# Optimization experiments

Hardware: AMD Instinct MI355X
Metric: run time of the kernel (lower is better)

The kernel has to match this reference:

```python
import jax, jax.numpy as jnp
import numpy as np

B, S, E, H = 2, 2048, 1024, 16
DH = E // H  # 64


def setup_inputs() -> dict:
    key = jax.random.key(0)
    ks = jax.random.split(key, 9)
    sc = 1.0 / np.sqrt(E)
    return {
        "x": jax.random.normal(ks[0], (B, S, E), dtype=jnp.float32),
        "Wq": jax.random.normal(ks[1], (E, E), dtype=jnp.float32) * sc,
        "bq": jax.random.normal(ks[2], (E,), dtype=jnp.float32) * 0.02,
        "Wk": jax.random.normal(ks[3], (E, E), dtype=jnp.float32) * sc,
        "bk": jax.random.normal(ks[4], (E,), dtype=jnp.float32) * 0.02,
        "Wv": jax.random.normal(ks[5], (E, E), dtype=jnp.float32) * sc,
        "bv": jax.random.normal(ks[6], (E,), dtype=jnp.float32) * 0.02,
        "Wo": jax.random.normal(ks[7], (E, E), dtype=jnp.float32) * sc,
        "bo": jax.random.normal(ks[8], (E,), dtype=jnp.float32) * 0.02,
    }


def reference(x, Wq, bq, Wk, bk, Wv, bv, Wo, bo):
    b, s, e = x.shape
    h, dh = H, e // H
    # NOTE: original torch code does .view(B, H, S, Dh) on the [B, S, E]
    # projection WITHOUT transposing first; we replicate that exact reshape.
    q = (x @ Wq.T + bq).reshape(b, h, s, dh)
    k = (x @ Wk.T + bk).reshape(b, h, s, dh)
    v = (x @ Wv.T + bv).reshape(b, h, s, dh)
    scale = 1.0 / jnp.sqrt(jnp.asarray(dh, dtype=x.dtype))
    scores = jax.nn.softmax(jnp.einsum("bhqd,bhkd->bhqk", q, k) * scale, axis=-1)
    out = jnp.einsum("bhqk,bhkd->bhqd", scores, v)  # [B,H,S,Dh]
    out = out.transpose(0, 2, 1, 3).reshape(b, s, e)  # matches torch transpose(1,2).view
    return out @ Wo.T + bo
```

## Files before the change

### kernel.cpp

```cpp
#include <hip/hip_runtime.h>
#include <hip/hip_bf16.h>
#include <stdint.h>

typedef __bf16 bf16x8 __attribute__((ext_vector_type(8)));
typedef float  f32x4  __attribute__((ext_vector_type(4)));
typedef float  f32x16 __attribute__((ext_vector_type(16)));
typedef __hip_bfloat16 bf16;

__device__ __forceinline__ void gll16(const void* g, void* l) {
    typedef const unsigned int __attribute__((address_space(1)))* gp_t;
    typedef unsigned int __attribute__((address_space(3)))* lp_t;
    __builtin_amdgcn_global_load_lds((gp_t)(g), (lp_t)(l), 16, 0, 0);
}

__device__ __forceinline__ float fexp2(float x) {
#if __has_builtin(__builtin_amdgcn_exp2f)
    return __builtin_amdgcn_exp2f(x);
#else
    float r; asm volatile("v_exp_f32 %0, %1" : "=v"(r) : "v"(x)); return r;
#endif
}

__global__ __launch_bounds__(256) void prep_convert(
    const float* __restrict__ x,
    const float* __restrict__ wq, const float* __restrict__ wk,
    const float* __restrict__ wv, const float* __restrict__ wo,
    bf16* __restrict__ Xb, bf16* __restrict__ Wcat, bf16* __restrict__ Wob)
{
    int i = blockIdx.x * blockDim.x + threadIdx.x;
    int base = i * 4;
    const float* src; bf16* dst;
    if      (base < 4194304) { src = x  + base;             dst = Xb   + base; }
    else if (base < 5242880) { src = wq + (base - 4194304); dst = Wcat + (base - 4194304); }
    else if (base < 6291456) { src = wk + (base - 5242880); dst = Wcat + 1048576 + (base - 5242880); }
    else if (base < 7340032) { src = wv + (base - 6291456); dst = Wcat + 2097152 + (base - 6291456); }
    else                     { src = wo + (base - 7340032); dst = Wob  + (base - 7340032); }
    float4 v = *(const float4*)src;
    union { bf16 h[4]; ushort4 u; } cv;
    cv.h[0] = __float2bfloat16(v.x);
    cv.h[1] = __float2bfloat16(v.y);
    cv.h[2] = __float2bfloat16(v.z);
    cv.h[3] = __float2bfloat16(v.w);
    *(ushort4*)dst = cv.u;
}

__global__ __launch_bounds__(256, 2) void gemm_qkv(
    const bf16* __restrict__ X, const bf16* __restrict__ Wc,
    const float* __restrict__ bq, const float* __restrict__ bk, const float* __restrict__ bv,
    bf16* __restrict__ Pq, bf16* __restrict__ Pk, bf16* __restrict__ Pv)
{
    __shared__ __align__(16) bf16 Ab[128 * 32];
    __shared__ __align__(16) bf16 Bb[128 * 32];
    const int t = threadIdx.x;
    const int lane = t & 63, w = t >> 6;
    const int lr = lane & 15, lg = lane >> 4;
    const int wr = w >> 1, wc = w & 1;
    const int row0 = blockIdx.y * 128, col0 = blockIdx.x * 128;

    f32x4 acc[4][4] = {};

    const char* Xc  = (const char*)X;
    const char* Wcc = (const char*)Wc;
    char* AbC = (char*)Ab;
    char* BbC = (char*)Bb;
    const int o0 = t * 16, o1 = o0 + 4096;
    const int ldsoff = w * 1024;

    for (int k0 = 0; k0 < 1024; k0 += 32) {
        __syncthreads();
        gll16(Xc  + (size_t)(row0 + (o0 >> 6)) * 2048 + (size_t)k0 * 2 + (o0 & 63), AbC + ldsoff);
        gll16(Wcc + (size_t)(col0 + (o0 >> 6)) * 2048 + (size_t)k0 * 2 + (o0 & 63), BbC + ldsoff);
        gll16(Xc  + (size_t)(row0 + (o1 >> 6)) * 2048 + (size_t)k0 * 2 + (o1 & 63), AbC + 4096 + ldsoff);
        gll16(Wcc + (size_t)(col0 + (o1 >> 6)) * 2048 + (size_t)k0 * 2 + (o1 & 63), BbC + 4096 + ldsoff);
        __syncthreads();
        bf16x8 af[4], bw[4];
        #pragma unroll
        for (int i = 0; i < 4; ++i)
            af[i] = *(const bf16x8*)(AbC + ((wr * 64 + i * 16 + lr) * 32 + lg * 8) * 2);
        #pragma unroll
        for (int j = 0; j < 4; ++j)
            bw[j] = *(const bf16x8*)(BbC + ((wc * 64 + j * 16 + lr) * 32 + lg * 8) * 2);
        #pragma unroll
        for (int i = 0; i < 4; ++i)
            #pragma unroll
            for (int j = 0; j < 4; ++j)
                acc[i][j] = __builtin_amdgcn_mfma_f32_16x16x32_bf16(af[i], bw[j], acc[i][j], 0, 0, 0);
    }

    const int mid = col0 >> 10;
    const float* bias = (mid == 0) ? bq : (mid == 1 ? bk : bv);
    bf16* Out = (mid == 0) ? Pq : (mid == 1 ? Pk : Pv);
    const float scale = (mid == 0) ? 0.125f * 1.44269504f : 1.0f;
    const int nc0 = col0 - (mid << 10) + wc * 64;
    const int mr0 = row0 + wr * 64;
    #pragma unroll
    for (int i = 0; i < 4; ++i)
        #pragma unroll
        for (int j = 0; j < 4; ++j) {
            int cc = nc0 + j * 16 + lr;
            float bsv = bias[cc];
            #pragma unroll
            for (int p = 0; p < 4; ++p) {
                int rr = mr0 + i * 16 + lg * 4 + p;
                Out[(size_t)rr * 1024 + cc] = __float2bfloat16((acc[i][j][p] + bsv) * scale);
            }
        }
}

__global__ __launch_bounds__(256) void transpose_v(const bf16* __restrict__ Pv, bf16* __restrict__ Vt)
{
    __shared__ bf16 tile[64][72];
    const int head = blockIdx.y;
    const int st   = blockIdx.x;
    const bf16* src = Pv + (size_t)head * 131072 + (size_t)st * 4096;
    bf16* dst = Vt + (size_t)head * 131072 + (size_t)st * 64;
    const int t = threadIdx.x;
    const int rr = t >> 2, c0 = (t & 3) * 16;
    #pragma unroll
    for (int u = 0; u < 2; ++u) {
        bf16x8 v = *(const bf16x8*)(src + rr * 64 + c0 + u * 8);
        #pragma unroll
        for (int e = 0; e < 8; ++e) tile[rr][c0 + u * 8 + e] = ((const bf16*)&v)[e];
    }
    __syncthreads();
    #pragma unroll
    for (int u = 0; u < 2; ++u) {
        bf16 ov[8];
        #pragma unroll
        for (int e = 0; e < 8; ++e) {
            int y = u * 8 + e;
            int z = (y & 3) | ((y & 8) >> 1) | ((y & 4) << 1);
            ov[e] = tile[c0 + z][rr];
        }
        *(bf16x8*)(dst + (size_t)rr * 2048 + c0 + u * 8) = *(const bf16x8*)ov;
    }
}

__global__ __launch_bounds__(256, 2) void attn_fwd(
    const bf16* __restrict__ Pq, const bf16* __restrict__ Pk,
    const bf16* __restrict__ Vt, bf16* __restrict__ Of)
{
    __shared__ __align__(16) bf16 Kl[2][128 * 64];
    __shared__ __align__(16) bf16 Vl[2][64 * 128];

    const int blk = blockIdx.x;
    const int head = blk >> 4;
    const int qt = blk & 15;
    const int bb = head >> 4, hh = head & 15;
    const bf16* Qh = Pq + (size_t)head * 131072;
    const char* Khc = (const char*)(Pk + (size_t)head * 131072);
    const char* Vhc = (const char*)(Vt + (size_t)head * 131072);

    const int t = threadIdx.x;
    const int lane = t & 63, w = t >> 6;
    const int ql = lane & 31, hi = lane >> 5;
    const int q0 = qt * 128 + w * 32;

    bf16x8 qf[4];
    #pragma unroll
    for (int m = 0; m < 4; ++m)
        qf[m] = *(const bf16x8*)(Qh + (size_t)(q0 + ql) * 64 + m * 16 + hi * 8);

    f32x16 acc[2] = {};
    float m_run = -1e30f, l_run = 0.f;

    const int stg_o   = t * 16;
    const int stg_key = stg_o >> 7, stg_ks = (stg_o >> 4) & 7;
    const int stg_d   = stg_o >> 8, stg_vs = (stg_o >> 4) & 15;
    const size_t kgo = (size_t)stg_key * 128 + ((stg_ks ^ (stg_key & 7)) * 16);
    const size_t vgo = (size_t)stg_d * 4096 + ((stg_vs ^ (stg_d & 7)) * 16);
    const int ldst = w * 1024;

#define STAGE(S0, BUF)                                                          \
    {                                                                           \
        char* KB = (char*)(Kl[BUF]);                                            \
        char* VB = (char*)(Vl[BUF]);                                            \
        _Pragma("unroll")                                                       \
        for (int qq = 0; qq < 4; ++qq) {                                        \
            gll16(Khc + (size_t)(S0) * 128 + (size_t)qq * 4096 + kgo,           \
                  KB + qq * 4096 + ldst);                                       \
            gll16(Vhc + (size_t)(S0) * 2 + (size_t)qq * 65536 + vgo,            \
                  VB + qq * 4096 + ldst);                                       \
        }                                                                       \
    }

    STAGE(0, 0);
    __syncthreads();

    int cur = 0;
    for (int s0 = 0; s0 < 2048; s0 += 128) {
        if (s0 + 128 < 2048) STAGE(s0 + 128, cur ^ 1);

        const char* KlC = (const char*)(Kl[cur]);
        const char* VlC = (const char*)(Vl[cur]);

        f32x16 sa[4] = {};
        __builtin_amdgcn_s_setprio(1);
        #pragma unroll
        for (int kb = 0; kb < 4; ++kb) {
            int row = kb * 32 + ql;
            #pragma unroll
            for (int m = 0; m < 4; ++m) {
                int byt = row * 128 + ((32 * m + 16 * hi) ^ ((row & 7) << 4));
                bf16x8 kf = *(const bf16x8*)(KlC + byt);
                sa[kb] = __builtin_amdgcn_mfma_f32_32x32x16_bf16(kf, qf[m], sa[kb], 0, 0, 0);
            }
        }
        __builtin_amdgcn_s_setprio(0);

        float mx = -1e30f;
        #pragma unroll
        for (int kb = 0; kb < 4; ++kb)
            #pragma unroll
            for (int r = 0; r < 16; ++r) mx = fmaxf(mx, sa[kb][r]);
        mx = fmaxf(mx, __shfl_xor(mx, 32));
        float mn = fmaxf(m_run, mx);
        float al = fexp2(m_run - mn);
        m_run = mn;
        float rs = 0.f;
        #pragma unroll
        for (int kb = 0; kb < 4; ++kb)
            #pragma unroll
            for (int r = 0; r < 16; ++r) {
                float p = fexp2(sa[kb][r] - mn);
                sa[kb][r] = p;
                rs += p;
            }
        rs += __shfl_xor(rs, 32);
        l_run = l_run * al + rs;
        #pragma unroll
        for (int r = 0; r < 16; ++r) { acc[0][r] *= al; acc[1][r] *= al; }

        __builtin_amdgcn_s_setprio(1);
        #pragma unroll
        for (int sb = 0; sb < 8; ++sb) {
            const int kb = sb >> 1, par = (sb & 1) * 8;
            bf16x8 pa;
            #pragma unroll
            for (int e = 0; e < 8; ++e) pa[e] = (__bf16)sa[kb][par + e];
            #pragma unroll
            for (int db = 0; db < 2; ++db) {
                int row = db * 32 + ql;
                int byt = row * 256 + ((sb * 32 + hi * 16) ^ ((row & 7) << 4));
                bf16x8 vf = *(const bf16x8*)(VlC + byt);
                acc[db] = __builtin_amdgcn_mfma_f32_32x32x16_bf16(vf, pa, acc[db], 0, 0, 0);
            }
        }
        __builtin_amdgcn_s_setprio(0);

        __syncthreads();
        cur ^= 1;
    }
#undef STAGE

    float inv = 1.0f / l_run;
    bf16* orow = Of + (size_t)(bb * 2048 + q0 + ql) * 1024 + hh * 64;
    #pragma unroll
    for (int db = 0; db < 2; ++db)
        #pragma unroll
        for (int g = 0; g < 4; ++g) {
            union { bf16 h[4]; ushort4 u; } ob;
            #pragma unroll
            for (int j = 0; j < 4; ++j)
                ob.h[j] = __float2bfloat16(acc[db][4 * g + j] * inv);
            *(ushort4*)(orow + db * 32 + 8 * g + 4 * hi) = ob.u;
        }
}

__global__ __launch_bounds__(256, 2) void gemm_out(
    const bf16* __restrict__ A, const bf16* __restrict__ W,
    const float* __restrict__ bo, float* __restrict__ C)
{
    __shared__ __align__(16) bf16 Ab[128 * 32];
    __shared__ __align__(16) bf16 Bb[128 * 32];
    const int t = threadIdx.x;
    const int lane = t & 63, w = t >> 6;
    const int lr = lane & 15, lg = lane >> 4;
    const int wr = w >> 1, wc = w & 1;
    const int row0 = blockIdx.y * 128, col0 = blockIdx.x * 128;

    f32x4 acc[4][4] = {};
    const char* Ac = (const char*)A;
    const char* Wc = (const char*)W;
    char* AbC = (char*)Ab;
    char* BbC = (char*)Bb;
    const int o0 = t * 16, o1 = o0 + 4096;
    const int ldsoff = w * 1024;

    for (int k0 = 0; k0 < 1024; k0 += 32) {
        __syncthreads();
        gll16(Ac + (size_t)(row0 + (o0 >> 6)) * 2048 + (size_t)k0 * 2 + (o0 & 63), AbC + ldsoff);
        gll16(Wc + (size_t)(col0 + (o0 >> 6)) * 2048 + (size_t)k0 * 2 + (o0 & 63), BbC + ldsoff);
        gll16(Ac + (size_t)(row0 + (o1 >> 6)) * 2048 + (size_t)k0 * 2 + (o1 & 63), AbC + 4096 + ldsoff);
        gll16(Wc + (size_t)(col0 + (o1 >> 6)) * 2048 + (size_t)k0 * 2 + (o1 & 63), BbC + 4096 + ldsoff);
        __syncthreads();
        bf16x8 af[4], bw[4];
        #pragma unroll
        for (int i = 0; i < 4; ++i)
            af[i] = *(const bf16x8*)(AbC + ((wr * 64 + i * 16 + lr) * 32 + lg * 8) * 2);
        #pragma unroll
        for (int j = 0; j < 4; ++j)
            bw[j] = *(const bf16x8*)(BbC + ((wc * 64 + j * 16 + lr) * 32 + lg * 8) * 2);
        #pragma unroll
        for (int i = 0; i < 4; ++i)
            #pragma unroll
            for (int j = 0; j < 4; ++j)
                acc[i][j] = __builtin_amdgcn_mfma_f32_16x16x32_bf16(af[i], bw[j], acc[i][j], 0, 0, 0);
    }

    const int nc0 = col0 + wc * 64;
    const int mr0 = row0 + wr * 64;
    #pragma unroll
    for (int i = 0; i < 4; ++i)
        #pragma unroll
        for (int j = 0; j < 4; ++j) {
            int cc = nc0 + j * 16 + lr;
            float bsv = bo[cc];
            #pragma unroll
            for (int p = 0; p < 4; ++p) {
                int rr = mr0 + i * 16 + lg * 4 + p;
                C[(size_t)rr * 1024 + cc] = acc[i][j][p] + bsv;
            }
        }
}

extern "C" void kernel_launch(void* const* d_in, const int* in_sizes, int n_in,
                              void* d_out, int out_size, void* d_ws, size_t ws_size,
                              hipStream_t stream) {
    const float* x  = (const float*)d_in[0];
    const float* Wq = (const float*)d_in[1];
    const float* bq = (const float*)d_in[2];
    const float* Wk = (const float*)d_in[3];
    const float* bk = (const float*)d_in[4];
    const float* Wv = (const float*)d_in[5];
    const float* bv = (const float*)d_in[6];
    const float* Wo = (const float*)d_in[7];
    const float* bo = (const float*)d_in[8];
    float* out = (float*)d_out;

    char* ws = (char*)d_ws;
    bf16* Xb   = (bf16*)(ws + 0);
    bf16* Wcat = (bf16*)(ws + 8388608);
    bf16* Wob  = (bf16*)(ws + 14680064);
    bf16* Pq   = (bf16*)(ws + 16777216);
    bf16* Pk   = (bf16*)(ws + 25165824);
    bf16* Pv   = (bf16*)(ws + 33554432);
    bf16* Vt   = (bf16*)(ws + 0);
    bf16* Of   = (bf16*)(ws + 33554432);
    (void)ws_size; (void)in_sizes; (void)n_in; (void)out_size;

    prep_convert<<<8192, 256, 0, stream>>>(x, Wq, Wk, Wv, Wo, Xb, Wcat, Wob);
    gemm_qkv<<<dim3(24, 32), 256, 0, stream>>>(Xb, Wcat, bq, bk, bv, Pq, Pk, Pv);
    transpose_v<<<dim3(32, 32), 256, 0, stream>>>(Pv, Vt);
    attn_fwd<<<512, 256, 0, stream>>>(Pq, Pk, Vt, Of);
    gemm_out<<<dim3(8, 32), 256, 0, stream>>>(Of, Wob, bo, out);
}
```

Before: 125.8 us.

## Remap block IDs for XCD locality and add lazy softmax rescaling

Linear block IDs are remapped so consecutive tiles land on the same XCD (stride-8 interleave) in the QKV GEMM, the attention kernel and the output GEMM. This is meant to improve L2 reuse of shared A/B tiles and K/V heads. The attention softmax also uses tree reductions for max and sum, and skips rescaling the running max and accumulator unless the new max exceeds the old one by more than 8 (log2 units). That removes per-tile exp and multiply work, at the risk of larger unnormalized values within the bounded threshold.

```diff
diff --git a/kernel.cpp b/kernel.cpp
--- a/kernel.cpp
+++ b/kernel.cpp
@@ -19,6 +19,24 @@
 #else
     float r; asm volatile("v_exp_f32 %0, %1" : "=v"(r) : "v"(x)); return r;
 #endif
+}
+
+__device__ __forceinline__ float tmax16(const f32x16& v) {
+    float a0 = fmaxf(v[0], v[1]),   a1 = fmaxf(v[2], v[3]);
+    float a2 = fmaxf(v[4], v[5]),   a3 = fmaxf(v[6], v[7]);
+    float a4 = fmaxf(v[8], v[9]),   a5 = fmaxf(v[10], v[11]);
+    float a6 = fmaxf(v[12], v[13]), a7 = fmaxf(v[14], v[15]);
+    float b0 = fmaxf(a0, a1), b1 = fmaxf(a2, a3);
+    float b2 = fmaxf(a4, a5), b3 = fmaxf(a6, a7);
+    return fmaxf(fmaxf(b0, b1), fmaxf(b2, b3));
+}
+__device__ __forceinline__ float tsum16(const f32x16& v) {
+    float a0 = v[0] + v[1],   a1 = v[2] + v[3];
+    float a2 = v[4] + v[5],   a3 = v[6] + v[7];
+    float a4 = v[8] + v[9],   a5 = v[10] + v[11];
+    float a6 = v[12] + v[13], a7 = v[14] + v[15];
+    float b0 = a0 + a1, b1 = a2 + a3, b2 = a4 + a5, b3 = a6 + a7;
+    return (b0 + b1) + (b2 + b3);
 }
 
 __global__ __launch_bounds__(256) void prep_convert(
@@ -51,11 +69,13 @@
 {
     __shared__ __align__(16) bf16 Ab[128 * 32];
     __shared__ __align__(16) bf16 Bb[128 * 32];
+    const int id = blockIdx.x;
+    const int sid = (id & 7) * 96 + (id >> 3);
     const int t = threadIdx.x;
     const int lane = t & 63, w = t >> 6;
     const int lr = lane & 15, lg = lane >> 4;
     const int wr = w >> 1, wc = w & 1;
-    const int row0 = blockIdx.y * 128, col0 = blockIdx.x * 128;
+    const int row0 = (sid / 24) * 128, col0 = (sid % 24) * 128;
 
     f32x4 acc[4][4] = {};
 
@@ -143,7 +163,8 @@
     __shared__ __align__(16) bf16 Kl[2][128 * 64];
     __shared__ __align__(16) bf16 Vl[2][64 * 128];
 
-    const int blk = blockIdx.x;
+    const int blk0 = blockIdx.x;
+    const int blk = (blk0 & 7) * 64 + (blk0 >> 3);
     const int head = blk >> 4;
     const int qt = blk & 15;
     const int bb = head >> 4, hh = head & 15;
@@ -208,28 +229,30 @@
         }
         __builtin_amdgcn_s_setprio(0);
 
-        float mx = -1e30f;
+        float mx = fmaxf(fmaxf(tmax16(sa[0]), tmax16(sa[1])),
+                         fmaxf(tmax16(sa[2]), tmax16(sa[3])));
+        mx = fmaxf(mx, __shfl_xor(mx, 32));
+
+        float mn;
+        if (__all(mx - m_run <= 8.0f)) {
+            mn = m_run;
+        } else {
+            mn = fmaxf(m_run, mx);
+            float al = fexp2(m_run - mn);
+            m_run = mn;
+            l_run *= al;
+            #pragma unroll
+            for (int r = 0; r < 16; ++r) { acc[0][r] *= al; acc[1][r] *= al; }
+        }
+
         #pragma unroll
         for (int kb = 0; kb < 4; ++kb)
             #pragma unroll
-            for (int r = 0; r < 16; ++r) mx = fmaxf(mx, sa[kb][r]);
-        mx = fmaxf(mx, __shfl_xor(mx, 32));
-        float mn = fmaxf(m_run, mx);
-        float al = fexp2(m_run - mn);
-        m_run = mn;
-        float rs = 0.f;
-        #pragma unroll
-        for (int kb = 0; kb < 4; ++kb)
-            #pragma unroll
-            for (int r = 0; r < 16; ++r) {
-                float p = fexp2(sa[kb][r] - mn);
-                sa[kb][r] = p;
-                rs += p;
-            }
+            for (int r = 0; r < 16; ++r)
+                sa[kb][r] = fexp2(sa[kb][r] - mn);
+        float rs = (tsum16(sa[0]) + tsum16(sa[1])) + (tsum16(sa[2]) + tsum16(sa[3]));
         rs += __shfl_xor(rs, 32);
-        l_run = l_run * al + rs;
-        #pragma unroll
-        for (int r = 0; r < 16; ++r) { acc[0][r] *= al; acc[1][r] *= al; }
+        l_run += rs;
 
         __builtin_amdgcn_s_setprio(1);
         #pragma unroll
@@ -273,11 +296,13 @@
 {
     __shared__ __align__(16) bf16 Ab[128 * 32];
     __shared__ __align__(16) bf16 Bb[128 * 32];
+    const int id = blockIdx.x;
+    const int sid = (id & 7) * 32 + (id >> 3);
     const int t = threadIdx.x;
     const int lane = t & 63, w = t >> 6;
     const int lr = lane & 15, lg = lane >> 4;
     const int wr = w >> 1, wc = w & 1;
-    const int row0 = blockIdx.y * 128, col0 = blockIdx.x * 128;
+    const int row0 = (sid / 8) * 128, col0 = (sid % 8) * 128;
 
     f32x4 acc[4][4] = {};
     const char* Ac = (const char*)A;
@@ -350,8 +375,8 @@
     (void)ws_size; (void)in_sizes; (void)n_in; (void)out_size;
 
     prep_convert<<<8192, 256, 0, stream>>>(x, Wq, Wk, Wv, Wo, Xb, Wcat, Wob);
-    gemm_qkv<<<dim3(24, 32), 256, 0, stream>>>(Xb, Wcat, bq, bk, bv, Pq, Pk, Pv);
+    gemm_qkv<<<768, 256, 0, stream>>>(Xb, Wcat, bq, bk, bv, Pq, Pk, Pv);
     transpose_v<<<dim3(32, 32), 256, 0, stream>>>(Pv, Vt);
     attn_fwd<<<512, 256, 0, stream>>>(Pq, Pk, Vt, Of);
-    gemm_out<<<dim3(8, 32), 256, 0, stream>>>(Of, Wob, bo, out);
-}
+    gemm_out<<<256, 256, 0, stream>>>(Of, Wob, bo, out);
+}
```

New measurement: 123.5 us. No clear change (-1.8%).
